# Kernel optimization log

Hardware: AMD Instinct MI355X
Metric: run time of the kernel (lower is better)

Reference implementation:

```python
import jax, jax.numpy as jnp
import numpy as np

N = 50000          # number of parent nodes / neighborhoods
D_IN = 256         # input_size
K = 8              # points decoded per neighborhood
GLOBAL_DIMS = [256, 128, 64]
FC_DIMS = [256, 256, 256]


def _linear_params(key, d_in, d_out):
    kw, kb = jax.random.split(key)
    W = jax.random.normal(kw, (d_in, d_out), dtype=jnp.float32) * 0.05
    b = jax.random.normal(kb, (d_out,), dtype=jnp.float32) * 0.05
    return W, b


def setup_inputs() -> dict:
    key = jax.random.key(0)
    keys = jax.random.split(key, 8)
    inp = {"input_features": jax.random.normal(keys[0], (N, D_IN), dtype=jnp.float32)}
    # global MLP: 256 -> 256 -> 128 -> 64
    d = D_IN
    for i, nb in enumerate(GLOBAL_DIMS):
        W, b = _linear_params(keys[1 + i], d, nb)
        inp[f"Wg{i}"], inp[f"bg{i}"] = W, b
        d = nb
    # neighborhood decoder head: 64 -> K*3
    inp["Wdec"], inp["bdec"] = _linear_params(keys[4], GLOBAL_DIMS[-1], K * 3)
    # per-point MLP: (256 + 64 + 3) -> 256 -> 256 -> 256
    d = D_IN + GLOBAL_DIMS[-1] + 3
    for i, nb in enumerate(FC_DIMS):
        W, b = _linear_params(keys[5 + i], d, nb)
        inp[f"W{i}"], inp[f"b{i}"] = W, b
        d = nb
    return inp


def reference(input_features, Wg0, bg0, Wg1, bg1, Wg2, bg2, Wdec, bdec,
              W0, b0, W1, b1, W2, b2):
    relu = jax.nn.relu
    # global feature MLP on node features: [N, 256] -> [N, 64]
    feats = input_features
    for W, b in ((Wg0, bg0), (Wg1, bg1), (Wg2, bg2)):
        feats = relu(feats @ W + b)
    # neighborhood decoder: K relative 3D points per node -> [N*K, 3]
    relative_points = (feats @ Wdec + bdec).reshape(-1, 3)
    cluster = jnp.repeat(jnp.arange(N, dtype=jnp.int32), K)  # [N*K]
    # gather (duplicate) parent features per decoded point
    nbr_dup = jnp.take(feats, cluster, axis=0)               # [N*K, 64]
    inp_dup = jnp.take(input_features, cluster, axis=0)      # [N*K, 256]
    decoded = jnp.concatenate([inp_dup, nbr_dup, relative_points], axis=1)  # [N*K, 323]
    for W, b in ((W0, b0), (W1, b1), (W2, b2)):
        decoded = relu(decoded @ W + b)
    return relative_points, decoded, cluster
```

## Files before the change

### kernel.cpp

```cpp
#include <hip/hip_runtime.h>
#include <hip/hip_bf16.h>

typedef __attribute__((ext_vector_type(8))) __bf16 bf16x8;
typedef __attribute__((ext_vector_type(4))) float f32x4;
typedef __attribute__((ext_vector_type(4))) unsigned short u16x4;

#define NN 50000
#define TM1 16
#define NODES2 8


#define FEATS_OFF 212992
#define GW_OFF    3412992

__device__ __forceinline__ unsigned short f2bf(float f) {
    unsigned int u = __builtin_bit_cast(unsigned int, f);
    u = (u + 0x7FFFu + ((u >> 16) & 1u)) >> 16;
    return (unsigned short)u;
}
__device__ __forceinline__ float bf2f(unsigned short h) {
    return __builtin_bit_cast(float, (unsigned int)h << 16);
}

__global__ __launch_bounds__(256) void k_prep(
    const float* __restrict__ W0, const float* __restrict__ W1,
    const float* __restrict__ W2,
    const float* __restrict__ Wg0, const float* __restrict__ Wg1,
    const float* __restrict__ Wg2,
    unsigned short* __restrict__ wbf)
{
    int idx = blockIdx.x * 256 + threadIdx.x;
    if (idx < 81920) {
        int n = idx / 320, k = idx - n * 320;
        wbf[idx] = f2bf(W0[(size_t)k * 256 + n]);
    } else if (idx < 147456) {
        int e = idx - 81920;
        int n = e >> 8, k = e & 255;
        wbf[idx] = f2bf(W1[(size_t)k * 256 + n]);
    } else if (idx < 212992) {
        int e = idx - 147456;
        int n = e >> 8, k = e & 255;
        wbf[idx] = f2bf(W2[(size_t)k * 256 + n]);
    } else if (idx < 319488) {
        int e = idx - 212992;
        float v; int oh, ol;
        if (e < 65536) {
            int n = e >> 8, k = e & 255;
            v = Wg0[(size_t)k * 256 + n];
            oh = GW_OFF + e; ol = GW_OFF + 65536 + e;
        } else if (e < 98304) {
            int e2 = e - 65536;
            int n = e2 >> 8, k = e2 & 255;
            v = Wg1[(size_t)k * 128 + n];
            oh = GW_OFF + 131072 + e2; ol = GW_OFF + 163840 + e2;
        } else {
            int e3 = e - 98304;
            int n = e3 >> 7, k = e3 & 127;
            v = Wg2[(size_t)k * 64 + n];
            oh = GW_OFF + 196608 + e3; ol = GW_OFF + 204800 + e3;
        }
        unsigned short h = f2bf(v);
        wbf[oh] = h;
        wbf[ol] = f2bf(v - bf2f(h));
    }
}

__global__ __launch_bounds__(256) void k_global(
    const float* __restrict__ x,
    const float* __restrict__ bg0, const float* __restrict__ bg1,
    const float* __restrict__ bg2,
    const float* __restrict__ Wdec, const float* __restrict__ bdec,
    const unsigned short* __restrict__ gw,
    unsigned short* __restrict__ feats_bf,
    float* __restrict__ out_rel,
    float* __restrict__ out_cluster)
{
    __shared__ __attribute__((aligned(16))) unsigned short xh[TM1 * 264];
    __shared__ __attribute__((aligned(16))) unsigned short xl[TM1 * 264];
    __shared__ __attribute__((aligned(16))) unsigned short hh[TM1 * 264];
    __shared__ __attribute__((aligned(16))) unsigned short hl[TM1 * 264];
    __shared__ __attribute__((aligned(16))) unsigned short q1h[TM1 * 136];
    __shared__ __attribute__((aligned(16))) unsigned short q1l[TM1 * 136];
    __shared__ __attribute__((aligned(16))) float g2[TM1 * 64];

    const int tid  = threadIdx.x;
    const int lane = tid & 63;
    const int w    = tid >> 6;
    const int quad = lane >> 4;
    const int l15  = lane & 15;
    const int blk  = blockIdx.x;

    for (int e = tid; e < TM1 * 256; e += 256) {
        int r = e >> 8, c = e & 255;
        float v = x[(size_t)(blk * TM1 + r) * 256 + c];
        unsigned short h = f2bf(v);
        xh[r * 264 + c] = h;
        xl[r * 264 + c] = f2bf(v - bf2f(h));
    }
    __syncthreads();

    {
        const unsigned short* Wh = gw;
        const unsigned short* Wl = gw + 65536;
        f32x4 acc[4];
        f32x4 z = {0.f, 0.f, 0.f, 0.f};
        #pragma unroll
        for (int t = 0; t < 4; ++t) acc[t] = z;
        for (int ks = 0; ks < 8; ++ks) {
            int k0 = ks * 32 + quad * 8;
            bf16x8 ah = *(const bf16x8*)&xh[l15 * 264 + k0];
            bf16x8 al = *(const bf16x8*)&xl[l15 * 264 + k0];
            #pragma unroll
            for (int t = 0; t < 4; ++t) {
                int n = w * 64 + t * 16 + l15;
                bf16x8 bh = *(const bf16x8*)(Wh + (size_t)n * 256 + k0);
                bf16x8 bl = *(const bf16x8*)(Wl + (size_t)n * 256 + k0);
                acc[t] = __builtin_amdgcn_mfma_f32_16x16x32_bf16(ah, bh, acc[t], 0, 0, 0);
                acc[t] = __builtin_amdgcn_mfma_f32_16x16x32_bf16(al, bh, acc[t], 0, 0, 0);
                acc[t] = __builtin_amdgcn_mfma_f32_16x16x32_bf16(ah, bl, acc[t], 0, 0, 0);
            }
        }
        #pragma unroll
        for (int t = 0; t < 4; ++t) {
            int col = w * 64 + t * 16 + l15;
            float bb = bg0[col];
            #pragma unroll
            for (int r = 0; r < 4; ++r) {
                int row = quad * 4 + r;
                float v = fmaxf(acc[t][r] + bb, 0.f);
                unsigned short h = f2bf(v);
                hh[row * 264 + col] = h;
                hl[row * 264 + col] = f2bf(v - bf2f(h));
            }
        }
    }
    __syncthreads();

    {
        const unsigned short* Wh = gw + 131072;
        const unsigned short* Wl = gw + 163840;
        f32x4 acc[2];
        f32x4 z = {0.f, 0.f, 0.f, 0.f};
        acc[0] = z; acc[1] = z;
        for (int ks = 0; ks < 8; ++ks) {
            int k0 = ks * 32 + quad * 8;
            bf16x8 ah = *(const bf16x8*)&hh[l15 * 264 + k0];
            bf16x8 al = *(const bf16x8*)&hl[l15 * 264 + k0];
            #pragma unroll
            for (int t = 0; t < 2; ++t) {
                int n = w * 32 + t * 16 + l15;
                bf16x8 bh = *(const bf16x8*)(Wh + (size_t)n * 256 + k0);
                bf16x8 bl = *(const bf16x8*)(Wl + (size_t)n * 256 + k0);
                acc[t] = __builtin_amdgcn_mfma_f32_16x16x32_bf16(ah, bh, acc[t], 0, 0, 0);
                acc[t] = __builtin_amdgcn_mfma_f32_16x16x32_bf16(al, bh, acc[t], 0, 0, 0);
                acc[t] = __builtin_amdgcn_mfma_f32_16x16x32_bf16(ah, bl, acc[t], 0, 0, 0);
            }
        }
        #pragma unroll
        for (int t = 0; t < 2; ++t) {
            int col = w * 32 + t * 16 + l15;
            float bb = bg1[col];
            #pragma unroll
            for (int r = 0; r < 4; ++r) {
                int row = quad * 4 + r;
                float v = fmaxf(acc[t][r] + bb, 0.f);
                unsigned short h = f2bf(v);
                q1h[row * 136 + col] = h;
                q1l[row * 136 + col] = f2bf(v - bf2f(h));
            }
        }
    }
    __syncthreads();

    {
        const unsigned short* Wh = gw + 196608;
        const unsigned short* Wl = gw + 204800;
        f32x4 acc = {0.f, 0.f, 0.f, 0.f};
        for (int ks = 0; ks < 4; ++ks) {
            int k0 = ks * 32 + quad * 8;
            bf16x8 ah = *(const bf16x8*)&q1h[l15 * 136 + k0];
            bf16x8 al = *(const bf16x8*)&q1l[l15 * 136 + k0];
            int n = w * 16 + l15;
            bf16x8 bh = *(const bf16x8*)(Wh + (size_t)n * 128 + k0);
            bf16x8 bl = *(const bf16x8*)(Wl + (size_t)n * 128 + k0);
            acc = __builtin_amdgcn_mfma_f32_16x16x32_bf16(ah, bh, acc, 0, 0, 0);
            acc = __builtin_amdgcn_mfma_f32_16x16x32_bf16(al, bh, acc, 0, 0, 0);
            acc = __builtin_amdgcn_mfma_f32_16x16x32_bf16(ah, bl, acc, 0, 0, 0);
        }
        int col = w * 16 + l15;
        float bb = bg2[col];
        #pragma unroll
        for (int r = 0; r < 4; ++r) {
            int row = quad * 4 + r;
            g2[row * 64 + col] = fmaxf(acc[r] + bb, 0.f);
        }
    }
    __syncthreads();

    {
        const float* src = g2 + tid * 4;
        u16x4 p;
        p[0] = f2bf(src[0]); p[1] = f2bf(src[1]);
        p[2] = f2bf(src[2]); p[3] = f2bf(src[3]);
        *(u16x4*)&feats_bf[(size_t)blk * (TM1 * 64) + tid * 4] = p;
    }

    for (int tt = tid; tt < TM1 * 24; tt += 256) {
        int m = tt / 24;
        int c = tt - m * 24;
        float acc = bdec[c];
        for (int i = 0; i < 64; ++i) acc += g2[m * 64 + i] * Wdec[i * 24 + c];
        out_rel[(size_t)blk * (TM1 * 24) + tt] = acc;
    }

    if (tid < TM1 * 8) {
        out_cluster[(size_t)blk * (TM1 * 8) + tid] = (float)(blk * TM1 + (tid >> 3));
    }
}

__global__ __launch_bounds__(256) void k_points(
    const float* __restrict__ x,
    const unsigned short* __restrict__ feats_bf,
    const float* __restrict__ rel_in,
    const unsigned short* __restrict__ wbf,
    const float* __restrict__ W0f,
    const float* __restrict__ b0,
    const float* __restrict__ b1,
    const float* __restrict__ b2,
    float* __restrict__ out_dec)
{
    __shared__ __attribute__((aligned(16))) unsigned short h0s[64 * 264];
    __shared__ __attribute__((aligned(16))) unsigned short h1s[64 * 264];
    __shared__ __attribute__((aligned(16))) unsigned short xcat[NODES2 * 336];
    __shared__ __attribute__((aligned(16))) float w3buf[3 * 256];
    __shared__ __attribute__((aligned(16))) float rl[NODES2 * 24];
    float* s = (float*)h1s;

    const int tid  = threadIdx.x;
    const int lane = tid & 63;
    const int w    = tid >> 6;
    const int quad = lane >> 4;
    const int l15  = lane & 15;
    const int blk  = blockIdx.x;
    const size_t nb = (size_t)blk * NODES2;

    for (int e = tid; e < NODES2 * 256; e += 256) {
        int r = e >> 8, c = e & 255;
        xcat[r * 336 + c] = f2bf(x[(nb + r) * 256 + c]);
    }
    {
        int e = tid * 2;
        int r = e >> 6, c = e & 63;
        *(unsigned int*)&xcat[r * 336 + 256 + c] =
            *(const unsigned int*)&feats_bf[nb * 64 + e];
    }
    for (int e = tid; e < 3 * 256; e += 256) {
        int r = e >> 8, c = e & 255;
        w3buf[e] = W0f[(size_t)(320 + r) * 256 + c];
    }
    if (tid < NODES2 * 24) rl[tid] = rel_in[nb * 24 + tid];
    __syncthreads();

    {
        const unsigned short* W0t = wbf;
        f32x4 acc[4];
        f32x4 z = {0.f, 0.f, 0.f, 0.f};
        #pragma unroll
        for (int t = 0; t < 4; ++t) acc[t] = z;
        const unsigned short* arow = &xcat[(lane & 7) * 336];
        for (int ks = 0; ks < 10; ++ks) {
            int k0 = ks * 32 + quad * 8;
            bf16x8 a = *(const bf16x8*)(arow + k0);
            #pragma unroll
            for (int t = 0; t < 4; ++t) {
                int n = w * 64 + t * 16 + l15;
                bf16x8 b = *(const bf16x8*)(W0t + (size_t)n * 320 + k0);
                acc[t] = __builtin_amdgcn_mfma_f32_16x16x32_bf16(a, b, acc[t], 0, 0, 0);
            }
        }
        #pragma unroll
        for (int t = 0; t < 4; ++t) {
            int col = w * 64 + t * 16 + l15;
            float bb = b0[col];
            #pragma unroll
            for (int r = 0; r < 4; ++r) {
                int row = quad * 4 + r;
                if (row < NODES2) s[row * 256 + col] = acc[t][r] + bb;
            }
        }
    }
    __syncthreads();

    for (int it = 0; it < 16; ++it) {
        int task = tid + it * 256;
        int row = task >> 6;
        int cg  = task & 63;
        int node = row >> 3, p = row & 7;
        float4 sv = *(const float4*)&s[node * 256 + cg * 4];
        float ra = rl[node * 24 + p * 3 + 0];
        float rb = rl[node * 24 + p * 3 + 1];
        float rc = rl[node * 24 + p * 3 + 2];
        float4 wa = *(const float4*)&w3buf[cg * 4];
        float4 wbv = *(const float4*)&w3buf[256 + cg * 4];
        float4 wc = *(const float4*)&w3buf[512 + cg * 4];
        float v0 = fmaxf(sv.x + ra * wa.x + rb * wbv.x + rc * wc.x, 0.f);
        float v1 = fmaxf(sv.y + ra * wa.y + rb * wbv.y + rc * wc.y, 0.f);
        float v2 = fmaxf(sv.z + ra * wa.z + rb * wbv.z + rc * wc.z, 0.f);
        float v3 = fmaxf(sv.w + ra * wa.w + rb * wbv.w + rc * wc.w, 0.f);
        unsigned int lo = (unsigned int)f2bf(v0) | ((unsigned int)f2bf(v1) << 16);
        unsigned int hi = (unsigned int)f2bf(v2) | ((unsigned int)f2bf(v3) << 16);
        uint2 pk; pk.x = lo; pk.y = hi;
        *(uint2*)&h0s[row * 264 + cg * 4] = pk;
    }
    __syncthreads();

    {
        const unsigned short* W1t = wbf + 81920;
        f32x4 acc[4][4];
        f32x4 z = {0.f, 0.f, 0.f, 0.f};
        #pragma unroll
        for (int m = 0; m < 4; ++m)
            #pragma unroll
            for (int t = 0; t < 4; ++t) acc[m][t] = z;
        for (int ks = 0; ks < 8; ++ks) {
            int k0 = ks * 32 + quad * 8;
            bf16x8 a[4], b[4];
            #pragma unroll
            for (int m = 0; m < 4; ++m)
                a[m] = *(const bf16x8*)&h0s[(m * 16 + l15) * 264 + k0];
            #pragma unroll
            for (int t = 0; t < 4; ++t)
                b[t] = *(const bf16x8*)(W1t + (size_t)(w * 64 + t * 16 + l15) * 256 + k0);
            #pragma unroll
            for (int m = 0; m < 4; ++m)
                #pragma unroll
                for (int t = 0; t < 4; ++t)
                    acc[m][t] = __builtin_amdgcn_mfma_f32_16x16x32_bf16(a[m], b[t], acc[m][t], 0, 0, 0);
        }
        #pragma unroll
        for (int t = 0; t < 4; ++t) {
            int col = w * 64 + t * 16 + l15;
            float bb = b1[col];
            #pragma unroll
            for (int m = 0; m < 4; ++m) {
                #pragma unroll
                for (int r = 0; r < 4; ++r) {
                    int row = m * 16 + quad * 4 + r;
                    h1s[row * 264 + col] = f2bf(fmaxf(acc[m][t][r] + bb, 0.f));
                }
            }
        }
    }
    __syncthreads();

    {
        const unsigned short* W2t = wbf + 147456;
        f32x4 acc[4][4];
        f32x4 z = {0.f, 0.f, 0.f, 0.f};
        #pragma unroll
        for (int m = 0; m < 4; ++m)
            #pragma unroll
            for (int t = 0; t < 4; ++t) acc[m][t] = z;
        for (int ks = 0; ks < 8; ++ks) {
            int k0 = ks * 32 + quad * 8;
            bf16x8 a[4], b[4];
            #pragma unroll
            for (int m = 0; m < 4; ++m)
                a[m] = *(const bf16x8*)&h1s[(m * 16 + l15) * 264 + k0];
            #pragma unroll
            for (int t = 0; t < 4; ++t)
                b[t] = *(const bf16x8*)(W2t + (size_t)(w * 64 + t * 16 + l15) * 256 + k0);
            #pragma unroll
            for (int m = 0; m < 4; ++m)
                #pragma unroll
                for (int t = 0; t < 4; ++t)
                    acc[m][t] = __builtin_amdgcn_mfma_f32_16x16x32_bf16(a[m], b[t], acc[m][t], 0, 0, 0);
        }
        #pragma unroll
        for (int t = 0; t < 4; ++t) {
            int col = w * 64 + t * 16 + l15;
            float bb = b2[col];
            #pragma unroll
            for (int m = 0; m < 4; ++m) {
                #pragma unroll
                for (int r = 0; r < 4; ++r) {
                    int row = m * 16 + quad * 4 + r;
                    out_dec[(nb * 8 + row) * 256 + col] = fmaxf(acc[m][t][r] + bb, 0.f);
                }
            }
        }
    }
}

extern "C" void kernel_launch(void* const* d_in, const int* in_sizes, int n_in,
                              void* d_out, int out_size, void* d_ws, size_t ws_size,
                              hipStream_t stream) {
    const float* x    = (const float*)d_in[0];
    const float* Wg0  = (const float*)d_in[1];
    const float* bg0  = (const float*)d_in[2];
    const float* Wg1  = (const float*)d_in[3];
    const float* bg1  = (const float*)d_in[4];
    const float* Wg2  = (const float*)d_in[5];
    const float* bg2  = (const float*)d_in[6];
    const float* Wdec = (const float*)d_in[7];
    const float* bdec = (const float*)d_in[8];
    const float* W0   = (const float*)d_in[9];
    const float* b0   = (const float*)d_in[10];
    const float* W1   = (const float*)d_in[11];
    const float* b1   = (const float*)d_in[12];
    const float* W2   = (const float*)d_in[13];
    const float* b2   = (const float*)d_in[14];

    float* out      = (float*)d_out;
    float* out_rel  = out;
    float* out_dec  = out + 1200000;
    float* out_clu  = out + 103600000;

    unsigned short* wbf      = (unsigned short*)d_ws;
    unsigned short* feats_bf = wbf + FEATS_OFF;
    unsigned short* gw       = wbf + GW_OFF;

    k_prep<<<1248, 256, 0, stream>>>(W0, W1, W2, Wg0, Wg1, Wg2, wbf);
    k_global<<<NN / TM1, 256, 0, stream>>>(x, bg0, bg1, bg2, Wdec, bdec, gw,
                                           feats_bf, out_rel, out_clu);
    k_points<<<NN / NODES2, 256, 0, stream>>>(x, feats_bf, out_rel,
                                              wbf, W0, b0, b1, b2, out_dec);
}
```

Measured before the change: 979.2 us.

## Fuse global MLP and per-point MLP into one kernel with swizzled shared buffers

Merges the global-feature kernel and the per-point kernel into a single kernel that processes 8 nodes per block. Intermediate feats and relative points stay in shared memory instead of going through a global workspace, and x is read once. Shared memory is aliased and the hidden activations use an XOR-swizzled layout in a single buffer, which cuts LDS use so that 3 blocks can fit per CU. The cost is that the global-MLP MFMAs now run half-empty (only 8 of 16 rows are valid), and an extra barrier is needed so the in-place hidden buffer can be reused safely.

```diff
diff --git a/kernel.cpp b/kernel.cpp
--- a/kernel.cpp
+++ b/kernel.cpp
@@ -6,12 +6,9 @@
 typedef __attribute__((ext_vector_type(4))) unsigned short u16x4;
 
 #define NN 50000
-#define TM1 16
-#define NODES2 8
-
-
-#define FEATS_OFF 212992
-#define GW_OFF    3412992
+#define NODES 8
+
+#define GW_OFF 212992
 
 __device__ __forceinline__ unsigned short f2bf(float f) {
     unsigned int u = __builtin_bit_cast(unsigned int, f);
@@ -65,23 +62,31 @@
     }
 }
 
-__global__ __launch_bounds__(256) void k_global(
+__global__ __launch_bounds__(256, 3) void k_fused(
     const float* __restrict__ x,
     const float* __restrict__ bg0, const float* __restrict__ bg1,
     const float* __restrict__ bg2,
     const float* __restrict__ Wdec, const float* __restrict__ bdec,
-    const unsigned short* __restrict__ gw,
-    unsigned short* __restrict__ feats_bf,
-    float* __restrict__ out_rel,
-    float* __restrict__ out_cluster)
+    const unsigned short* __restrict__ wbf,
+    const float* __restrict__ W0f,
+    const float* __restrict__ b0, const float* __restrict__ b1,
+    const float* __restrict__ b2,
+    float* __restrict__ out_rel, float* __restrict__ out_clu,
+    float* __restrict__ out_dec)
 {
-    __shared__ __attribute__((aligned(16))) unsigned short xh[TM1 * 264];
-    __shared__ __attribute__((aligned(16))) unsigned short xl[TM1 * 264];
-    __shared__ __attribute__((aligned(16))) unsigned short hh[TM1 * 264];
-    __shared__ __attribute__((aligned(16))) unsigned short hl[TM1 * 264];
-    __shared__ __attribute__((aligned(16))) unsigned short q1h[TM1 * 136];
-    __shared__ __attribute__((aligned(16))) unsigned short q1l[TM1 * 136];
-    __shared__ __attribute__((aligned(16))) float g2[TM1 * 64];
+    __shared__ __attribute__((aligned(16))) unsigned char smem[53760];
+    unsigned short* xh  = (unsigned short*)(smem);
+    unsigned short* xl  = (unsigned short*)(smem + 4224);
+    unsigned short* q1h = (unsigned short*)(smem + 4224);
+    unsigned short* q1l = (unsigned short*)(smem + 6400);
+    float*          w3  = (float*)(smem + 4224);
+    unsigned short* gh  = (unsigned short*)(smem + 8576);
+    unsigned short* gl  = (unsigned short*)(smem + 12800);
+    float*          sP  = (float*)(smem + 8576);
+    float*          g2  = (float*)(smem + 17024);
+    unsigned short* fb  = (unsigned short*)(smem + 19072);
+    float*          rl  = (float*)(smem + 20224);
+    unsigned char*  hB  = smem + 20992;
 
     const int tid  = threadIdx.x;
     const int lane = tid & 63;
@@ -89,27 +94,38 @@
     const int quad = lane >> 4;
     const int l15  = lane & 15;
     const int blk  = blockIdx.x;
-
-    for (int e = tid; e < TM1 * 256; e += 256) {
-        int r = e >> 8, c = e & 255;
-        float v = x[(size_t)(blk * TM1 + r) * 256 + c];
-        unsigned short h = f2bf(v);
-        xh[r * 264 + c] = h;
-        xl[r * 264 + c] = f2bf(v - bf2f(h));
-    }
-    __syncthreads();
-
-    {
-        const unsigned short* Wh = gw;
-        const unsigned short* Wl = gw + 65536;
+    const size_t nb = (size_t)blk * NODES;
+
+    {
+        const float4* xg = (const float4*)(x + nb * 256);
+        #pragma unroll
+        for (int it = 0; it < 2; ++it) {
+            int e = tid + it * 256;
+            int r = e >> 6, c4 = e & 63;
+            float4 v = xg[e];
+            u16x4 hv, lv;
+            hv[0] = f2bf(v.x); lv[0] = f2bf(v.x - bf2f(hv[0]));
+            hv[1] = f2bf(v.y); lv[1] = f2bf(v.y - bf2f(hv[1]));
+            hv[2] = f2bf(v.z); lv[2] = f2bf(v.z - bf2f(hv[2]));
+            hv[3] = f2bf(v.w); lv[3] = f2bf(v.w - bf2f(hv[3]));
+            *(u16x4*)&xh[r * 264 + c4 * 4] = hv;
+            *(u16x4*)&xl[r * 264 + c4 * 4] = lv;
+        }
+    }
+    __syncthreads();
+
+    {
+        const unsigned short* Wh = wbf + GW_OFF;
+        const unsigned short* Wl = Wh + 65536;
         f32x4 acc[4];
         f32x4 z = {0.f, 0.f, 0.f, 0.f};
         #pragma unroll
         for (int t = 0; t < 4; ++t) acc[t] = z;
+        const int ar = (l15 & 7) * 264;
         for (int ks = 0; ks < 8; ++ks) {
             int k0 = ks * 32 + quad * 8;
-            bf16x8 ah = *(const bf16x8*)&xh[l15 * 264 + k0];
-            bf16x8 al = *(const bf16x8*)&xl[l15 * 264 + k0];
+            bf16x8 ah = *(const bf16x8*)&xh[ar + k0];
+            bf16x8 al = *(const bf16x8*)&xl[ar + k0];
             #pragma unroll
             for (int t = 0; t < 4; ++t) {
                 int n = w * 64 + t * 16 + l15;
@@ -127,25 +143,28 @@
             #pragma unroll
             for (int r = 0; r < 4; ++r) {
                 int row = quad * 4 + r;
-                float v = fmaxf(acc[t][r] + bb, 0.f);
-                unsigned short h = f2bf(v);
-                hh[row * 264 + col] = h;
-                hl[row * 264 + col] = f2bf(v - bf2f(h));
-            }
-        }
-    }
-    __syncthreads();
-
-    {
-        const unsigned short* Wh = gw + 131072;
-        const unsigned short* Wl = gw + 163840;
+                if (row < 8) {
+                    float v = fmaxf(acc[t][r] + bb, 0.f);
+                    unsigned short hv = f2bf(v);
+                    gh[row * 264 + col] = hv;
+                    gl[row * 264 + col] = f2bf(v - bf2f(hv));
+                }
+            }
+        }
+    }
+    __syncthreads();
+
+    {
+        const unsigned short* Wh = wbf + GW_OFF + 131072;
+        const unsigned short* Wl = wbf + GW_OFF + 163840;
         f32x4 acc[2];
         f32x4 z = {0.f, 0.f, 0.f, 0.f};
         acc[0] = z; acc[1] = z;
+        const int ar = (l15 & 7) * 264;
         for (int ks = 0; ks < 8; ++ks) {
             int k0 = ks * 32 + quad * 8;
-            bf16x8 ah = *(const bf16x8*)&hh[l15 * 264 + k0];
-            bf16x8 al = *(const bf16x8*)&hl[l15 * 264 + k0];
+            bf16x8 ah = *(const bf16x8*)&gh[ar + k0];
+            bf16x8 al = *(const bf16x8*)&gl[ar + k0];
             #pragma unroll
             for (int t = 0; t < 2; ++t) {
                 int n = w * 32 + t * 16 + l15;
@@ -163,23 +182,26 @@
             #pragma unroll
             for (int r = 0; r < 4; ++r) {
                 int row = quad * 4 + r;
-                float v = fmaxf(acc[t][r] + bb, 0.f);
-                unsigned short h = f2bf(v);
-                q1h[row * 136 + col] = h;
-                q1l[row * 136 + col] = f2bf(v - bf2f(h));
-            }
-        }
-    }
-    __syncthreads();
-
-    {
-        const unsigned short* Wh = gw + 196608;
-        const unsigned short* Wl = gw + 204800;
+                if (row < 8) {
+                    float v = fmaxf(acc[t][r] + bb, 0.f);
+                    unsigned short hv = f2bf(v);
+                    q1h[row * 136 + col] = hv;
+                    q1l[row * 136 + col] = f2bf(v - bf2f(hv));
+                }
+            }
+        }
+    }
+    __syncthreads();
+
+    {
+        const unsigned short* Wh = wbf + GW_OFF + 196608;
+        const unsigned short* Wl = wbf + GW_OFF + 204800;
         f32x4 acc = {0.f, 0.f, 0.f, 0.f};
+        const int ar = (l15 & 7) * 136;
         for (int ks = 0; ks < 4; ++ks) {
             int k0 = ks * 32 + quad * 8;
-            bf16x8 ah = *(const bf16x8*)&q1h[l15 * 136 + k0];
-            bf16x8 al = *(const bf16x8*)&q1l[l15 * 136 + k0];
+            bf16x8 ah = *(const bf16x8*)&q1h[ar + k0];
+            bf16x8 al = *(const bf16x8*)&q1l[ar + k0];
             int n = w * 16 + l15;
             bf16x8 bh = *(const bf16x8*)(Wh + (size_t)n * 128 + k0);
             bf16x8 bl = *(const bf16x8*)(Wl + (size_t)n * 128 + k0);
@@ -192,73 +214,28 @@
         #pragma unroll
         for (int r = 0; r < 4; ++r) {
             int row = quad * 4 + r;
-            g2[row * 64 + col] = fmaxf(acc[r] + bb, 0.f);
-        }
-    }
-    __syncthreads();
-
-    {
-        const float* src = g2 + tid * 4;
-        u16x4 p;
-        p[0] = f2bf(src[0]); p[1] = f2bf(src[1]);
-        p[2] = f2bf(src[2]); p[3] = f2bf(src[3]);
-        *(u16x4*)&feats_bf[(size_t)blk * (TM1 * 64) + tid * 4] = p;
-    }
-
-    for (int tt = tid; tt < TM1 * 24; tt += 256) {
-        int m = tt / 24;
-        int c = tt - m * 24;
-        float acc = bdec[c];
-        for (int i = 0; i < 64; ++i) acc += g2[m * 64 + i] * Wdec[i * 24 + c];
-        out_rel[(size_t)blk * (TM1 * 24) + tt] = acc;
-    }
-
-    if (tid < TM1 * 8) {
-        out_cluster[(size_t)blk * (TM1 * 8) + tid] = (float)(blk * TM1 + (tid >> 3));
-    }
-}
-
-__global__ __launch_bounds__(256) void k_points(
-    const float* __restrict__ x,
-    const unsigned short* __restrict__ feats_bf,
-    const float* __restrict__ rel_in,
-    const unsigned short* __restrict__ wbf,
-    const float* __restrict__ W0f,
-    const float* __restrict__ b0,
-    const float* __restrict__ b1,
-    const float* __restrict__ b2,
-    float* __restrict__ out_dec)
-{
-    __shared__ __attribute__((aligned(16))) unsigned short h0s[64 * 264];
-    __shared__ __attribute__((aligned(16))) unsigned short h1s[64 * 264];
-    __shared__ __attribute__((aligned(16))) unsigned short xcat[NODES2 * 336];
-    __shared__ __attribute__((aligned(16))) float w3buf[3 * 256];
-    __shared__ __attribute__((aligned(16))) float rl[NODES2 * 24];
-    float* s = (float*)h1s;
-
-    const int tid  = threadIdx.x;
-    const int lane = tid & 63;
-    const int w    = tid >> 6;
-    const int quad = lane >> 4;
-    const int l15  = lane & 15;
-    const int blk  = blockIdx.x;
-    const size_t nb = (size_t)blk * NODES2;
-
-    for (int e = tid; e < NODES2 * 256; e += 256) {
-        int r = e >> 8, c = e & 255;
-        xcat[r * 336 + c] = f2bf(x[(nb + r) * 256 + c]);
-    }
-    {
-        int e = tid * 2;
-        int r = e >> 6, c = e & 63;
-        *(unsigned int*)&xcat[r * 336 + 256 + c] =
-            *(const unsigned int*)&feats_bf[nb * 64 + e];
-    }
-    for (int e = tid; e < 3 * 256; e += 256) {
-        int r = e >> 8, c = e & 255;
-        w3buf[e] = W0f[(size_t)(320 + r) * 256 + c];
-    }
-    if (tid < NODES2 * 24) rl[tid] = rel_in[nb * 24 + tid];
+            if (row < 8) {
+                float v = fmaxf(acc[r] + bb, 0.f);
+                g2[row * 64 + col] = v;
+                fb[row * 72 + col] = f2bf(v);
+            }
+        }
+    }
+    __syncthreads();
+
+    {
+        for (int e = tid; e < 768; e += 256)
+            w3[e] = W0f[(size_t)(320 + (e >> 8)) * 256 + (e & 255)];
+        if (tid < 192) {
+            int m = tid / 24, c = tid - m * 24;
+            float acc = bdec[c];
+            for (int i = 0; i < 64; ++i) acc += g2[m * 64 + i] * Wdec[i * 24 + c];
+            out_rel[(size_t)blk * 192 + tid] = acc;
+            rl[tid] = acc;
+        }
+        if (tid < 64)
+            out_clu[(size_t)blk * 64 + tid] = (float)(blk * 8 + (tid >> 3));
+    }
     __syncthreads();
 
     {
@@ -267,10 +244,10 @@
         f32x4 z = {0.f, 0.f, 0.f, 0.f};
         #pragma unroll
         for (int t = 0; t < 4; ++t) acc[t] = z;
-        const unsigned short* arow = &xcat[(lane & 7) * 336];
-        for (int ks = 0; ks < 10; ++ks) {
-            int k0 = ks * 32 + quad * 8;
-            bf16x8 a = *(const bf16x8*)(arow + k0);
+        const int ar8 = lane & 7;
+        for (int ks = 0; ks < 8; ++ks) {
+            int k0 = ks * 32 + quad * 8;
+            bf16x8 a = *(const bf16x8*)&xh[ar8 * 264 + k0];
             #pragma unroll
             for (int t = 0; t < 4; ++t) {
                 int n = w * 64 + t * 16 + l15;
@@ -279,13 +256,24 @@
             }
         }
         #pragma unroll
+        for (int ks = 8; ks < 10; ++ks) {
+            int k0 = ks * 32 + quad * 8;
+            bf16x8 a = *(const bf16x8*)&fb[ar8 * 72 + (k0 - 256)];
+            #pragma unroll
+            for (int t = 0; t < 4; ++t) {
+                int n = w * 64 + t * 16 + l15;
+                bf16x8 b = *(const bf16x8*)(W0t + (size_t)n * 320 + k0);
+                acc[t] = __builtin_amdgcn_mfma_f32_16x16x32_bf16(a, b, acc[t], 0, 0, 0);
+            }
+        }
+        #pragma unroll
         for (int t = 0; t < 4; ++t) {
             int col = w * 64 + t * 16 + l15;
             float bb = b0[col];
             #pragma unroll
             for (int r = 0; r < 4; ++r) {
                 int row = quad * 4 + r;
-                if (row < NODES2) s[row * 256 + col] = acc[t][r] + bb;
+                if (row < 8) sP[row * 256 + col] = acc[t][r] + bb;
             }
         }
     }
@@ -296,13 +284,13 @@
         int row = task >> 6;
         int cg  = task & 63;
         int node = row >> 3, p = row & 7;
-        float4 sv = *(const float4*)&s[node * 256 + cg * 4];
+        float4 sv = *(const float4*)&sP[node * 256 + cg * 4];
         float ra = rl[node * 24 + p * 3 + 0];
         float rb = rl[node * 24 + p * 3 + 1];
         float rc = rl[node * 24 + p * 3 + 2];
-        float4 wa = *(const float4*)&w3buf[cg * 4];
-        float4 wbv = *(const float4*)&w3buf[256 + cg * 4];
-        float4 wc = *(const float4*)&w3buf[512 + cg * 4];
+        float4 wa  = *(const float4*)&w3[cg * 4];
+        float4 wbv = *(const float4*)&w3[256 + cg * 4];
+        float4 wc  = *(const float4*)&w3[512 + cg * 4];
         float v0 = fmaxf(sv.x + ra * wa.x + rb * wbv.x + rc * wc.x, 0.f);
         float v1 = fmaxf(sv.y + ra * wa.y + rb * wbv.y + rc * wc.y, 0.f);
         float v2 = fmaxf(sv.z + ra * wa.z + rb * wbv.z + rc * wc.z, 0.f);
@@ -310,7 +298,8 @@
         unsigned int lo = (unsigned int)f2bf(v0) | ((unsigned int)f2bf(v1) << 16);
         unsigned int hi = (unsigned int)f2bf(v2) | ((unsigned int)f2bf(v3) << 16);
         uint2 pk; pk.x = lo; pk.y = hi;
-        *(uint2*)&h0s[row * 264 + cg * 4] = pk;
+        int byteoff = row * 512 + ((((cg >> 1) ^ (row & 7)) << 4) | ((cg & 1) << 3));
+        *(uint2*)(hB + byteoff) = pk;
     }
     __syncthreads();
 
@@ -324,10 +313,13 @@
             for (int t = 0; t < 4; ++t) acc[m][t] = z;
         for (int ks = 0; ks < 8; ++ks) {
             int k0 = ks * 32 + quad * 8;
+            int g  = k0 >> 3;
             bf16x8 a[4], b[4];
             #pragma unroll
-            for (int m = 0; m < 4; ++m)
-                a[m] = *(const bf16x8*)&h0s[(m * 16 + l15) * 264 + k0];
+            for (int m = 0; m < 4; ++m) {
+                int row = m * 16 + l15;
+                a[m] = *(const bf16x8*)(hB + row * 512 + ((g ^ (row & 7)) << 4));
+            }
             #pragma unroll
             for (int t = 0; t < 4; ++t)
                 b[t] = *(const bf16x8*)(W1t + (size_t)(w * 64 + t * 16 + l15) * 256 + k0);
@@ -337,6 +329,7 @@
                 for (int t = 0; t < 4; ++t)
                     acc[m][t] = __builtin_amdgcn_mfma_f32_16x16x32_bf16(a[m], b[t], acc[m][t], 0, 0, 0);
         }
+        __syncthreads();
         #pragma unroll
         for (int t = 0; t < 4; ++t) {
             int col = w * 64 + t * 16 + l15;
@@ -346,7 +339,10 @@
                 #pragma unroll
                 for (int r = 0; r < 4; ++r) {
                     int row = m * 16 + quad * 4 + r;
-                    h1s[row * 264 + col] = f2bf(fmaxf(acc[m][t][r] + bb, 0.f));
+                    int byteoff = row * 512 +
+                        ((((col >> 3) ^ (row & 7)) << 4) | ((col & 7) << 1));
+                    *(unsigned short*)(hB + byteoff) =
+                        f2bf(fmaxf(acc[m][t][r] + bb, 0.f));
                 }
             }
         }
@@ -363,10 +359,13 @@
             for (int t = 0; t < 4; ++t) acc[m][t] = z;
         for (int ks = 0; ks < 8; ++ks) {
             int k0 = ks * 32 + quad * 8;
+            int g  = k0 >> 3;
             bf16x8 a[4], b[4];
             #pragma unroll
-            for (int m = 0; m < 4; ++m)
-                a[m] = *(const bf16x8*)&h1s[(m * 16 + l15) * 264 + k0];
+            for (int m = 0; m < 4; ++m) {
+                int row = m * 16 + l15;
+                a[m] = *(const bf16x8*)(hB + row * 512 + ((g ^ (row & 7)) << 4));
+            }
             #pragma unroll
             for (int t = 0; t < 4; ++t)
                 b[t] = *(const bf16x8*)(W2t + (size_t)(w * 64 + t * 16 + l15) * 256 + k0);
@@ -385,7 +384,8 @@
                 #pragma unroll
                 for (int r = 0; r < 4; ++r) {
                     int row = m * 16 + quad * 4 + r;
-                    out_dec[(nb * 8 + row) * 256 + col] = fmaxf(acc[m][t][r] + bb, 0.f);
+                    out_dec[((size_t)blk * 64 + row) * 256 + col] =
+                        fmaxf(acc[m][t][r] + bb, 0.f);
                 }
             }
         }
@@ -416,13 +416,10 @@
     float* out_dec  = out + 1200000;
     float* out_clu  = out + 103600000;
 
-    unsigned short* wbf      = (unsigned short*)d_ws;
-    unsigned short* feats_bf = wbf + FEATS_OFF;
-    unsigned short* gw       = wbf + GW_OFF;
+    unsigned short* wbf = (unsigned short*)d_ws;
 
     k_prep<<<1248, 256, 0, stream>>>(W0, W1, W2, Wg0, Wg1, Wg2, wbf);
-    k_global<<<NN / TM1, 256, 0, stream>>>(x, bg0, bg1, bg2, Wdec, bdec, gw,
-                                           feats_bf, out_rel, out_clu);
-    k_points<<<NN / NODES2, 256, 0, stream>>>(x, feats_bf, out_rel,
-                                              wbf, W0, b0, b1, b2, out_dec);
+    k_fused<<<NN / NODES, 256, 0, stream>>>(x, bg0, bg1, bg2, Wdec, bdec,
+                                            wbf, W0, b0, b1, b2,
+                                            out_rel, out_clu, out_dec);
 }
```

New measurement: 1.034 ms. +5.6%, slower.

## Enlarge point-MLP tiles to 16 nodes with 512 threads and swizzled shared buffers

Applied to the files above, without the earlier changes.

The per-point MLP kernel now handles 16 nodes (128 points) per block with 8 waves arranged 2x4, so each weight fragment loaded from global memory serves twice as many rows. The first-layer GEMM now fills all 16 MFMA rows instead of 8. Shared buffers are aliased into one XOR-swizzled region to cut LDS footprint and bank conflicts, which needs an extra barrier before the in-place overwrite. The global kernel also aliases its LDS, vectorizes its input load with float4, and gets an occupancy hint. The trade-off is more LDS per block (~70KB) and higher register pressure, which may limit occupancy.

```diff
diff --git a/kernel.cpp b/kernel.cpp
--- a/kernel.cpp
+++ b/kernel.cpp
@@ -7,8 +7,7 @@
 
 #define NN 50000
 #define TM1 16
-#define NODES2 8
-
+#define PNODES 16
 
 #define FEATS_OFF 212992
 #define GW_OFF    3412992
@@ -65,7 +64,7 @@
     }
 }
 
-__global__ __launch_bounds__(256) void k_global(
+__global__ __launch_bounds__(256, 4) void k_global(
     const float* __restrict__ x,
     const float* __restrict__ bg0, const float* __restrict__ bg1,
     const float* __restrict__ bg2,
@@ -75,13 +74,14 @@
     float* __restrict__ out_rel,
     float* __restrict__ out_cluster)
 {
-    __shared__ __attribute__((aligned(16))) unsigned short xh[TM1 * 264];
-    __shared__ __attribute__((aligned(16))) unsigned short xl[TM1 * 264];
-    __shared__ __attribute__((aligned(16))) unsigned short hh[TM1 * 264];
-    __shared__ __attribute__((aligned(16))) unsigned short hl[TM1 * 264];
-    __shared__ __attribute__((aligned(16))) unsigned short q1h[TM1 * 136];
-    __shared__ __attribute__((aligned(16))) unsigned short q1l[TM1 * 136];
-    __shared__ __attribute__((aligned(16))) float g2[TM1 * 64];
+    __shared__ __attribute__((aligned(16))) unsigned char smem[37888];
+    unsigned short* xh  = (unsigned short*)(smem);
+    unsigned short* xl  = (unsigned short*)(smem + 8448);
+    unsigned short* q1h = (unsigned short*)(smem);
+    unsigned short* q1l = (unsigned short*)(smem + 4352);
+    unsigned short* hh  = (unsigned short*)(smem + 16896);
+    unsigned short* hl  = (unsigned short*)(smem + 25344);
+    float*          g2  = (float*)(smem + 33792);
 
     const int tid  = threadIdx.x;
     const int lane = tid & 63;
@@ -90,12 +90,21 @@
     const int l15  = lane & 15;
     const int blk  = blockIdx.x;
 
-    for (int e = tid; e < TM1 * 256; e += 256) {
-        int r = e >> 8, c = e & 255;
-        float v = x[(size_t)(blk * TM1 + r) * 256 + c];
-        unsigned short h = f2bf(v);
-        xh[r * 264 + c] = h;
-        xl[r * 264 + c] = f2bf(v - bf2f(h));
+    {
+        const float4* xg = (const float4*)(x + (size_t)blk * TM1 * 256);
+        #pragma unroll
+        for (int it = 0; it < 4; ++it) {
+            int e = tid + it * 256;
+            int r = e >> 6, c4 = e & 63;
+            float4 v = xg[e];
+            u16x4 hv, lv;
+            hv[0] = f2bf(v.x); lv[0] = f2bf(v.x - bf2f(hv[0]));
+            hv[1] = f2bf(v.y); lv[1] = f2bf(v.y - bf2f(hv[1]));
+            hv[2] = f2bf(v.z); lv[2] = f2bf(v.z - bf2f(hv[2]));
+            hv[3] = f2bf(v.w); lv[3] = f2bf(v.w - bf2f(hv[3]));
+            *(u16x4*)&xh[r * 264 + c4 * 4] = hv;
+            *(u16x4*)&xl[r * 264 + c4 * 4] = lv;
+        }
     }
     __syncthreads();
 
@@ -218,7 +227,7 @@
     }
 }
 
-__global__ __launch_bounds__(256) void k_points(
+__global__ __launch_bounds__(512, 4) void k_points(
     const float* __restrict__ x,
     const unsigned short* __restrict__ feats_bf,
     const float* __restrict__ rel_in,
@@ -229,88 +238,102 @@
     const float* __restrict__ b2,
     float* __restrict__ out_dec)
 {
-    __shared__ __attribute__((aligned(16))) unsigned short h0s[64 * 264];
-    __shared__ __attribute__((aligned(16))) unsigned short h1s[64 * 264];
-    __shared__ __attribute__((aligned(16))) unsigned short xcat[NODES2 * 336];
-    __shared__ __attribute__((aligned(16))) float w3buf[3 * 256];
-    __shared__ __attribute__((aligned(16))) float rl[NODES2 * 24];
-    float* s = (float*)h1s;
+    __shared__ __attribute__((aligned(16))) unsigned char smem[70144];
+    unsigned char*  hB   = smem;
+    unsigned short* xcat = (unsigned short*)smem;
+    float*          sp   = (float*)(smem + 49152);
+    float*          w3   = (float*)(smem + 65536);
+    float*          rl   = (float*)(smem + 68608);
 
     const int tid  = threadIdx.x;
     const int lane = tid & 63;
     const int w    = tid >> 6;
+    const int wr   = w >> 2;
+    const int wc   = w & 3;
     const int quad = lane >> 4;
     const int l15  = lane & 15;
     const int blk  = blockIdx.x;
-    const size_t nb = (size_t)blk * NODES2;
-
-    for (int e = tid; e < NODES2 * 256; e += 256) {
-        int r = e >> 8, c = e & 255;
-        xcat[r * 336 + c] = f2bf(x[(nb + r) * 256 + c]);
-    }
-    {
-        int e = tid * 2;
-        int r = e >> 6, c = e & 63;
-        *(unsigned int*)&xcat[r * 336 + 256 + c] =
-            *(const unsigned int*)&feats_bf[nb * 64 + e];
-    }
-    for (int e = tid; e < 3 * 256; e += 256) {
-        int r = e >> 8, c = e & 255;
-        w3buf[e] = W0f[(size_t)(320 + r) * 256 + c];
-    }
-    if (tid < NODES2 * 24) rl[tid] = rel_in[nb * 24 + tid];
+    const size_t nb = (size_t)blk * PNODES;
+
+    {
+        const float4* xg = (const float4*)(x + nb * 256);
+        #pragma unroll
+        for (int it = 0; it < 2; ++it) {
+            int e = tid + it * 512;
+            int r = e >> 6, c4 = e & 63;
+            float4 v = xg[e];
+            u16x4 hv;
+            hv[0] = f2bf(v.x); hv[1] = f2bf(v.y);
+            hv[2] = f2bf(v.z); hv[3] = f2bf(v.w);
+            *(u16x4*)&xcat[r * 336 + c4 * 4] = hv;
+        }
+        {
+            int e = tid * 2;
+            int r = e >> 6, c = e & 63;
+            *(unsigned int*)&xcat[r * 336 + 256 + c] =
+                *(const unsigned int*)&feats_bf[nb * 64 + e];
+        }
+        for (int e = tid; e < 768; e += 512)
+            w3[e] = W0f[(size_t)(320 + (e >> 8)) * 256 + (e & 255)];
+        if (tid < 384) rl[tid] = rel_in[nb * 24 + tid];
+    }
     __syncthreads();
 
     {
         const unsigned short* W0t = wbf;
-        f32x4 acc[4];
+        f32x4 acc[2];
         f32x4 z = {0.f, 0.f, 0.f, 0.f};
-        #pragma unroll
-        for (int t = 0; t < 4; ++t) acc[t] = z;
-        const unsigned short* arow = &xcat[(lane & 7) * 336];
+        acc[0] = z; acc[1] = z;
         for (int ks = 0; ks < 10; ++ks) {
             int k0 = ks * 32 + quad * 8;
-            bf16x8 a = *(const bf16x8*)(arow + k0);
-            #pragma unroll
-            for (int t = 0; t < 4; ++t) {
-                int n = w * 64 + t * 16 + l15;
+            bf16x8 a = *(const bf16x8*)&xcat[l15 * 336 + k0];
+            #pragma unroll
+            for (int t = 0; t < 2; ++t) {
+                int n = w * 32 + t * 16 + l15;
                 bf16x8 b = *(const bf16x8*)(W0t + (size_t)n * 320 + k0);
                 acc[t] = __builtin_amdgcn_mfma_f32_16x16x32_bf16(a, b, acc[t], 0, 0, 0);
             }
         }
         #pragma unroll
-        for (int t = 0; t < 4; ++t) {
-            int col = w * 64 + t * 16 + l15;
+        for (int t = 0; t < 2; ++t) {
+            int col = w * 32 + t * 16 + l15;
             float bb = b0[col];
             #pragma unroll
             for (int r = 0; r < 4; ++r) {
                 int row = quad * 4 + r;
-                if (row < NODES2) s[row * 256 + col] = acc[t][r] + bb;
-            }
-        }
-    }
-    __syncthreads();
-
-    for (int it = 0; it < 16; ++it) {
-        int task = tid + it * 256;
-        int row = task >> 6;
-        int cg  = task & 63;
-        int node = row >> 3, p = row & 7;
-        float4 sv = *(const float4*)&s[node * 256 + cg * 4];
-        float ra = rl[node * 24 + p * 3 + 0];
-        float rb = rl[node * 24 + p * 3 + 1];
-        float rc = rl[node * 24 + p * 3 + 2];
-        float4 wa = *(const float4*)&w3buf[cg * 4];
-        float4 wbv = *(const float4*)&w3buf[256 + cg * 4];
-        float4 wc = *(const float4*)&w3buf[512 + cg * 4];
-        float v0 = fmaxf(sv.x + ra * wa.x + rb * wbv.x + rc * wc.x, 0.f);
-        float v1 = fmaxf(sv.y + ra * wa.y + rb * wbv.y + rc * wc.y, 0.f);
-        float v2 = fmaxf(sv.z + ra * wa.z + rb * wbv.z + rc * wc.z, 0.f);
-        float v3 = fmaxf(sv.w + ra * wa.w + rb * wbv.w + rc * wc.w, 0.f);
-        unsigned int lo = (unsigned int)f2bf(v0) | ((unsigned int)f2bf(v1) << 16);
-        unsigned int hi = (unsigned int)f2bf(v2) | ((unsigned int)f2bf(v3) << 16);
-        uint2 pk; pk.x = lo; pk.y = hi;
-        *(uint2*)&h0s[row * 264 + cg * 4] = pk;
+                sp[row * 256 + col] = acc[t][r] + bb;
+            }
+        }
+    }
+    __syncthreads();
+
+    {
+        float4 sv0 = *(const float4*)&sp[(2 * w) * 256 + lane * 4];
+        float4 sv1 = *(const float4*)&sp[(2 * w + 1) * 256 + lane * 4];
+        float4 wa  = *(const float4*)&w3[lane * 4];
+        float4 wb4 = *(const float4*)&w3[256 + lane * 4];
+        float4 wc4 = *(const float4*)&w3[512 + lane * 4];
+        __syncthreads();
+        #pragma unroll
+        for (int it = 0; it < 16; ++it) {
+            int row  = w * 16 + it;
+            int node = 2 * w + (it >> 3);
+            int p    = it & 7;
+            float4 sv = (it < 8) ? sv0 : sv1;
+            float ra = rl[node * 24 + p * 3 + 0];
+            float rb = rl[node * 24 + p * 3 + 1];
+            float rc = rl[node * 24 + p * 3 + 2];
+            float v0 = fmaxf(sv.x + ra * wa.x + rb * wb4.x + rc * wc4.x, 0.f);
+            float v1 = fmaxf(sv.y + ra * wa.y + rb * wb4.y + rc * wc4.y, 0.f);
+            float v2 = fmaxf(sv.z + ra * wa.z + rb * wb4.z + rc * wc4.z, 0.f);
+            float v3 = fmaxf(sv.w + ra * wa.w + rb * wb4.w + rc * wc4.w, 0.f);
+            unsigned int lo = (unsigned int)f2bf(v0) | ((unsigned int)f2bf(v1) << 16);
+            unsigned int hi = (unsigned int)f2bf(v2) | ((unsigned int)f2bf(v3) << 16);
+            uint2 pk; pk.x = lo; pk.y = hi;
+            int byteoff = row * 512 +
+                ((((lane >> 1) ^ (row & 7)) << 4) | ((lane & 1) << 3));
+            *(uint2*)(hB + byteoff) = pk;
+        }
     }
     __syncthreads();
 
@@ -324,29 +347,36 @@
             for (int t = 0; t < 4; ++t) acc[m][t] = z;
         for (int ks = 0; ks < 8; ++ks) {
             int k0 = ks * 32 + quad * 8;
+            int g  = k0 >> 3;
             bf16x8 a[4], b[4];
             #pragma unroll
-            for (int m = 0; m < 4; ++m)
-                a[m] = *(const bf16x8*)&h0s[(m * 16 + l15) * 264 + k0];
+            for (int m = 0; m < 4; ++m) {
+                int row = wr * 64 + m * 16 + l15;
+                a[m] = *(const bf16x8*)(hB + row * 512 + ((g ^ (row & 7)) << 4));
+            }
             #pragma unroll
             for (int t = 0; t < 4; ++t)
-                b[t] = *(const bf16x8*)(W1t + (size_t)(w * 64 + t * 16 + l15) * 256 + k0);
+                b[t] = *(const bf16x8*)(W1t + (size_t)(wc * 64 + t * 16 + l15) * 256 + k0);
             #pragma unroll
             for (int m = 0; m < 4; ++m)
                 #pragma unroll
                 for (int t = 0; t < 4; ++t)
                     acc[m][t] = __builtin_amdgcn_mfma_f32_16x16x32_bf16(a[m], b[t], acc[m][t], 0, 0, 0);
         }
+        __syncthreads();
         #pragma unroll
         for (int t = 0; t < 4; ++t) {
-            int col = w * 64 + t * 16 + l15;
+            int col = wc * 64 + t * 16 + l15;
             float bb = b1[col];
             #pragma unroll
             for (int m = 0; m < 4; ++m) {
                 #pragma unroll
                 for (int r = 0; r < 4; ++r) {
-                    int row = m * 16 + quad * 4 + r;
-                    h1s[row * 264 + col] = f2bf(fmaxf(acc[m][t][r] + bb, 0.f));
+                    int row = wr * 64 + m * 16 + quad * 4 + r;
+                    int byteoff = row * 512 +
+                        ((((col >> 3) ^ (row & 7)) << 4) | ((col & 7) << 1));
+                    *(unsigned short*)(hB + byteoff) =
+                        f2bf(fmaxf(acc[m][t][r] + bb, 0.f));
                 }
             }
         }
@@ -363,13 +393,16 @@
             for (int t = 0; t < 4; ++t) acc[m][t] = z;
         for (int ks = 0; ks < 8; ++ks) {
             int k0 = ks * 32 + quad * 8;
+            int g  = k0 >> 3;
             bf16x8 a[4], b[4];
             #pragma unroll
-            for (int m = 0; m < 4; ++m)
-                a[m] = *(const bf16x8*)&h1s[(m * 16 + l15) * 264 + k0];
+            for (int m = 0; m < 4; ++m) {
+                int row = wr * 64 + m * 16 + l15;
+                a[m] = *(const bf16x8*)(hB + row * 512 + ((g ^ (row & 7)) << 4));
+            }
             #pragma unroll
             for (int t = 0; t < 4; ++t)
-                b[t] = *(const bf16x8*)(W2t + (size_t)(w * 64 + t * 16 + l15) * 256 + k0);
+                b[t] = *(const bf16x8*)(W2t + (size_t)(wc * 64 + t * 16 + l15) * 256 + k0);
             #pragma unroll
             for (int m = 0; m < 4; ++m)
                 #pragma unroll
@@ -378,14 +411,15 @@
         }
         #pragma unroll
         for (int t = 0; t < 4; ++t) {
-            int col = w * 64 + t * 16 + l15;
+            int col = wc * 64 + t * 16 + l15;
             float bb = b2[col];
             #pragma unroll
             for (int m = 0; m < 4; ++m) {
                 #pragma unroll
                 for (int r = 0; r < 4; ++r) {
-                    int row = m * 16 + quad * 4 + r;
-                    out_dec[(nb * 8 + row) * 256 + col] = fmaxf(acc[m][t][r] + bb, 0.f);
+                    int row = wr * 64 + m * 16 + quad * 4 + r;
+                    out_dec[((size_t)blk * 128 + row) * 256 + col] =
+                        fmaxf(acc[m][t][r] + bb, 0.f);
                 }
             }
         }
@@ -423,6 +457,6 @@
     k_prep<<<1248, 256, 0, stream>>>(W0, W1, W2, Wg0, Wg1, Wg2, wbf);
     k_global<<<NN / TM1, 256, 0, stream>>>(x, bg0, bg1, bg2, Wdec, bdec, gw,
                                            feats_bf, out_rel, out_clu);
-    k_points<<<NN / NODES2, 256, 0, stream>>>(x, feats_bf, out_rel,
+    k_points<<<NN / PNODES, 512, 0, stream>>>(x, feats_bf, out_rel,
                                               wbf, W0, b0, b1, b2, out_dec);
 }
```

Measured after the change: 878.6 us. -10.3%, faster.
